# Optimization experiments

Measured on AMD Instinct MI355X. Metric: run time of the kernel, lower is better.

Reference implementation:

```python
import jax, jax.numpy as jnp
import numpy as np

N_NODES = 50000
N_EDGES = 800000
N_IN = 96
N_HID = 96
N_CLS = 16
P_DROP = 0.5


def setup_inputs() -> dict:
    key = jax.random.key(0)
    ks = jax.random.split(key, 10)
    return {
        "features": jax.random.normal(ks[0], (N_NODES, N_IN), dtype=jnp.float32),
        "edge_weight": jax.random.uniform(ks[1], (N_EDGES,), dtype=jnp.float32),
        "src": jax.random.randint(ks[2], (N_EDGES,), 0, N_NODES),
        "dst": jax.random.randint(ks[3], (N_EDGES,), 0, N_NODES),
        "W0": jax.random.normal(ks[4], (N_IN, N_HID), dtype=jnp.float32) / np.sqrt(N_IN).astype(np.float32),
        "b0": jnp.zeros((N_HID,), dtype=jnp.float32),
        "W1": jax.random.normal(ks[5], (N_HID, N_HID), dtype=jnp.float32) / np.sqrt(N_HID).astype(np.float32),
        "b1": jnp.zeros((N_HID,), dtype=jnp.float32),
        "W2": jax.random.normal(ks[6], (N_HID, N_CLS), dtype=jnp.float32) / np.sqrt(N_HID).astype(np.float32),
        "b2": jnp.zeros((N_CLS,), dtype=jnp.float32),
    }


def reference(features, edge_weight, src, dst, W0, b0, W1, b1, W2, b2):
    N = features.shape[0]
    # Unweighted node degrees (DGL GraphConv norm='both'), clamped to >= 1.
    ones_e = jnp.ones_like(edge_weight)
    out_deg = jnp.clip(jax.ops.segment_sum(ones_e, src, num_segments=N), 1.0)
    in_deg = jnp.clip(jax.ops.segment_sum(ones_e, dst, num_segments=N), 1.0)
    inv_sqrt_out = out_deg ** -0.5  # [N]
    inv_sqrt_in = in_deg ** -0.5    # [N]

    def graph_conv(h, W, b, act):
        h = h * inv_sqrt_out[:, None]
        m = h[src] * edge_weight[:, None]                   # [E, d] gather + edge scale
        agg = jax.ops.segment_sum(m, dst, num_segments=N)   # [N, d] scatter-add
        out = (agg * inv_sqrt_in[:, None]) @ W + b          # D_in^-1/2, then linear + bias
        return act(out) if act is not None else out

    layers = [(W0, b0, jax.nn.relu), (W1, b1, jax.nn.relu), (W2, b2, None)]
    dkey = jax.random.key(42)
    h = features
    for i, (W, b, act) in enumerate(layers):
        keep = jax.random.bernoulli(jax.random.fold_in(dkey, i), 1.0 - P_DROP, h.shape)
        h = jnp.where(keep, h / (1.0 - P_DROP), 0.0)        # dropout p=0.5
        h = graph_conv(h, W, b, act)
    return jax.nn.log_softmax(h, axis=1)
```

## Files before the change

kernel.cpp:

```cpp
#include <hip/hip_runtime.h>
#include <hip/hip_fp16.h>
#include <stdint.h>

#define NNODES 50000
#define NEDGES 800000
#define NHID 96
#define NCLS 16

#define NC 100
#define NR 4
#define EPB (NEDGES / NC)
#define RNODES (NNODES / NR)
#define RWORDS8 (RNODES / 4)
#define NWORDS8 (NNODES / 4)
#define SCANB ((NWORDS8 + 255) / 256)
#define FILLBLKS (NC * NR)
#define NDROP4 ((NNODES * NHID / 4 + 255) / 256)

__host__ __device__ inline void tf2x32(uint32_t k0, uint32_t k1, uint32_t x0, uint32_t x1,
                                       uint32_t& o0, uint32_t& o1) {
  uint32_t k2 = k0 ^ k1 ^ 0x1BD11BDAu;
#define TFROT(v, r) (((v) << (r)) | ((v) >> (32 - (r))))
#define TFR(r) { x0 += x1; x1 = TFROT(x1, r); x1 ^= x0; }
  x0 += k0; x1 += k1;
  TFR(13) TFR(15) TFR(26) TFR(6)
  x0 += k1; x1 += k2 + 1u;
  TFR(17) TFR(29) TFR(16) TFR(24)
  x0 += k2; x1 += k0 + 2u;
  TFR(13) TFR(15) TFR(26) TFR(6)
  x0 += k0; x1 += k1 + 3u;
  TFR(17) TFR(29) TFR(16) TFR(24)
  x0 += k1; x1 += k2 + 4u;
  TFR(13) TFR(15) TFR(26) TFR(6)
  x0 += k2; x1 += k0 + 5u;
  o0 = x0; o1 = x1;
#undef TFR
#undef TFROT
}

__device__ inline bool keep_bit(uint32_t k0, uint32_t k1, uint32_t j) {
  uint32_t o0, o1;
  tf2x32(k0, k1, 0u, j, o0, o1);
  return (((o0 ^ o1) >> 31) == 0u);
}

__global__ __launch_bounds__(256) void hist_kernel(
    const int* __restrict__ src, const int* __restrict__ dst,
    uint32_t* __restrict__ slabD, uint32_t* __restrict__ slabS,
    uint32_t* __restrict__ flags) {
  __shared__ uint32_t HD[RWORDS8];
  __shared__ uint32_t HS[RWORDS8];
  const int tid = threadIdx.x, b = blockIdx.x;
  if (b == 0 && tid < SCANB) flags[tid] = 0;
  const int c = b / NR, r = b - c * NR;
  const int e0 = c * EPB, e1 = e0 + EPB;
  const int nbase = r * RNODES;
  for (int w = tid; w < RWORDS8; w += 256) { HD[w] = 0; HS[w] = 0; }
  __syncthreads();
  int e = e0 + tid;
  for (; e + 768 < e1; e += 1024) {
    int d0 = dst[e] - nbase,       d1 = dst[e + 256] - nbase;
    int d2 = dst[e + 512] - nbase, d3 = dst[e + 768] - nbase;
    int s0 = src[e] - nbase,       s1 = src[e + 256] - nbase;
    int s2 = src[e + 512] - nbase, s3 = src[e + 768] - nbase;
    if ((unsigned)d0 < (unsigned)RNODES) atomicAdd(&HD[d0 >> 2], 1u << ((d0 & 3) * 8));
    if ((unsigned)d1 < (unsigned)RNODES) atomicAdd(&HD[d1 >> 2], 1u << ((d1 & 3) * 8));
    if ((unsigned)d2 < (unsigned)RNODES) atomicAdd(&HD[d2 >> 2], 1u << ((d2 & 3) * 8));
    if ((unsigned)d3 < (unsigned)RNODES) atomicAdd(&HD[d3 >> 2], 1u << ((d3 & 3) * 8));
    if ((unsigned)s0 < (unsigned)RNODES) atomicAdd(&HS[s0 >> 2], 1u << ((s0 & 3) * 8));
    if ((unsigned)s1 < (unsigned)RNODES) atomicAdd(&HS[s1 >> 2], 1u << ((s1 & 3) * 8));
    if ((unsigned)s2 < (unsigned)RNODES) atomicAdd(&HS[s2 >> 2], 1u << ((s2 & 3) * 8));
    if ((unsigned)s3 < (unsigned)RNODES) atomicAdd(&HS[s3 >> 2], 1u << ((s3 & 3) * 8));
  }
  for (; e < e1; e += 256) {
    int d = dst[e] - nbase;
    if ((unsigned)d < (unsigned)RNODES) atomicAdd(&HD[d >> 2], 1u << ((d & 3) * 8));
    int s = src[e] - nbase;
    if ((unsigned)s < (unsigned)RNODES) atomicAdd(&HS[s >> 2], 1u << ((s & 3) * 8));
  }
  __syncthreads();
  uint32_t* dpD = slabD + (size_t)b * RWORDS8;
  uint32_t* dpS = slabS + (size_t)b * RWORDS8;
  for (int w = tid; w < RWORDS8; w += 256) { dpD[w] = HD[w]; dpS[w] = HS[w]; }
}

__global__ __launch_bounds__(256) void reduce_scan_kernel(
    const uint32_t* __restrict__ slabD, const uint32_t* __restrict__ slabS,
    float* __restrict__ inv_o, float* __restrict__ inv_i,
    uint32_t* __restrict__ rel8, int* __restrict__ row_ptr,
    uint32_t* __restrict__ flags) {
  __shared__ int lds[256];
  __shared__ int base_s;
  const int tid = threadIdx.x, b = blockIdx.x;
  const int gw = b * 256 + tid;
  uint32_t runD = 0, runS = 0;
  int n0 = 0;
  if (gw < NWORDS8) {
    int r = gw / RWORDS8, lw = gw - r * RWORDS8;
    n0 = r * RNODES + 4 * lw;
#pragma unroll 4
    for (int c = 0; c < NC; ++c) {
      rel8[(size_t)c * NWORDS8 + gw] = runD;
      runD += slabD[(size_t)(c * NR + r) * RWORDS8 + lw];
      runS += slabS[(size_t)(c * NR + r) * RWORDS8 + lw];
    }
  }
  const int d0 = runD & 0xFF, d1 = (runD >> 8) & 0xFF,
            d2 = (runD >> 16) & 0xFF, d3 = runD >> 24;
  const int tsum = d0 + d1 + d2 + d3;
  lds[tid] = tsum;
  __syncthreads();
  for (int off = 1; off < 256; off <<= 1) {
    int t = (tid >= off) ? lds[tid - off] : 0;
    __syncthreads();
    lds[tid] += t;
    __syncthreads();
  }
  const int incl = lds[tid];
  if (tid == 255) atomicExch(&flags[b], 0x80000000u | (uint32_t)lds[255]);
  if (tid < 64) {
    uint32_t part = 0;
    if (tid < b) {
      uint32_t v;
      do { v = atomicAdd(&flags[tid], 0u); } while (!(v & 0x80000000u));
      part = v & 0x7FFFFFFFu;
    }
#pragma unroll
    for (int off = 32; off > 0; off >>= 1)
      part += __shfl_down((unsigned)part, off, 64);
    if (tid == 0) base_s = (int)part;
  }
  __syncthreads();
  const int base = base_s;
  if (gw < NWORDS8) {
    int excl = base + incl - tsum;
    *(int4*)(row_ptr + n0) = make_int4(excl, excl + d0, excl + d0 + d1, excl + d0 + d1 + d2);
    *(float4*)(inv_i + n0) = make_float4(
        rsqrtf(fmaxf((float)d0, 1.0f)), rsqrtf(fmaxf((float)d1, 1.0f)),
        rsqrtf(fmaxf((float)d2, 1.0f)), rsqrtf(fmaxf((float)d3, 1.0f)));
    int o0 = runS & 0xFF, o1 = (runS >> 8) & 0xFF, o2 = (runS >> 16) & 0xFF, o3 = runS >> 24;
    *(float4*)(inv_o + n0) = make_float4(
        rsqrtf(fmaxf((float)o0, 1.0f)), rsqrtf(fmaxf((float)o1, 1.0f)),
        rsqrtf(fmaxf((float)o2, 1.0f)), rsqrtf(fmaxf((float)o3, 1.0f)));
    if (gw == NWORDS8 - 1) row_ptr[NNODES] = NEDGES;
  }
}

__global__ __launch_bounds__(256) void fill_drop_kernel(
    const int* __restrict__ src, const int* __restrict__ dst, const float* __restrict__ ew,
    const uint32_t* __restrict__ rel8, const int* __restrict__ row_ptr,
    uint32_t* __restrict__ csr,
    const float* __restrict__ h, const float* __restrict__ inv_o,
    float* __restrict__ X, uint32_t k0, uint32_t k1) {
  __shared__ uint32_t H[RWORDS8];
  const int tid = threadIdx.x, b = blockIdx.x;
  if (b >= FILLBLKS) {
    int j = ((b - FILLBLKS) * 256 + tid) * 4;
    if (j < NNODES * NHID) {
      int n = j / NHID;
      float4 hv = *(const float4*)(h + j);
      float sc = 2.0f * inv_o[n];
      float4 o;
      o.x = keep_bit(k0, k1, (uint32_t)(j + 0)) ? hv.x * sc : 0.0f;
      o.y = keep_bit(k0, k1, (uint32_t)(j + 1)) ? hv.y * sc : 0.0f;
      o.z = keep_bit(k0, k1, (uint32_t)(j + 2)) ? hv.z * sc : 0.0f;
      o.w = keep_bit(k0, k1, (uint32_t)(j + 3)) ? hv.w * sc : 0.0f;
      *(float4*)(X + j) = o;
    }
    return;
  }
  const int c = b / NR, r = b - c * NR;
  const int e0 = c * EPB, e1 = e0 + EPB;
  const int nbase = r * RNODES;
  const uint32_t* rel = rel8 + (size_t)c * NWORDS8;
  for (int w = tid; w < RWORDS8; w += 256) H[w] = 0;
  __syncthreads();
  int e = e0 + tid;
  for (; e + 256 < e1; e += 512) {
    int da = dst[e], db = dst[e + 256];
    int sa = src[e], sb = src[e + 256];
    float wa = ew[e], wb = ew[e + 256];
    int la = da - nbase, lb = db - nbase;
    bool ia = (unsigned)la < (unsigned)RNODES;
    bool ib = (unsigned)lb < (unsigned)RNODES;
    if (ia) {
      int sh = (la & 3) * 8;
      uint32_t old = atomicAdd(&H[la >> 2], 1u << sh);
      int rank = (int)((old >> sh) & 0xFFu);
      int rel_v = (int)((rel[da >> 2] >> sh) & 0xFFu);
      int pos = row_ptr[da] + rel_v + rank;
      if ((unsigned)pos < (unsigned)NEDGES) {
        uint32_t v = ((uint32_t)sa << 16) | (uint32_t)__half_as_ushort(__float2half_rn(wa));
        __builtin_nontemporal_store(v, &csr[pos]);
      }
    }
    if (ib) {
      int sh = (lb & 3) * 8;
      uint32_t old = atomicAdd(&H[lb >> 2], 1u << sh);
      int rank = (int)((old >> sh) & 0xFFu);
      int rel_v = (int)((rel[db >> 2] >> sh) & 0xFFu);
      int pos = row_ptr[db] + rel_v + rank;
      if ((unsigned)pos < (unsigned)NEDGES) {
        uint32_t v = ((uint32_t)sb << 16) | (uint32_t)__half_as_ushort(__float2half_rn(wb));
        __builtin_nontemporal_store(v, &csr[pos]);
      }
    }
  }
  for (; e < e1; e += 256) {
    int d = dst[e];
    int ld = d - nbase;
    if ((unsigned)ld < (unsigned)RNODES) {
      int sh = (ld & 3) * 8;
      uint32_t old = atomicAdd(&H[ld >> 2], 1u << sh);
      int rank = (int)((old >> sh) & 0xFFu);
      int rel_v = (int)((rel[d >> 2] >> sh) & 0xFFu);
      int pos = row_ptr[d] + rel_v + rank;
      if ((unsigned)pos < (unsigned)NEDGES) {
        uint32_t v = ((uint32_t)src[e] << 16) | (uint32_t)__half_as_ushort(__float2half_rn(ew[e]));
        __builtin_nontemporal_store(v, &csr[pos]);
      }
    }
  }
}

__global__ __launch_bounds__(256) void gemm96_kernel(
    const float* __restrict__ X, const float* __restrict__ W, __half* __restrict__ Yh) {
  __shared__ float Wl[96 * 96];
  const int tid = threadIdx.x;
  {
    const float4* Wg = (const float4*)W;
    float4* Ws = (float4*)Wl;
#pragma unroll
    for (int i = 0; i < 9; ++i)
      Ws[tid + i * 256] = Wg[tid + i * 256];
  }
  __syncthreads();

  const int cg = tid & 7;
  const int rq = tid >> 3;
  const int row0 = blockIdx.x * 128 + rq * 4;
  const int c0 = cg * 12;

  float acc[4][12];
#pragma unroll
  for (int r = 0; r < 4; ++r)
#pragma unroll
    for (int c = 0; c < 12; ++c) acc[r][c] = 0.f;

  const float* xr[4];
#pragma unroll
  for (int r = 0; r < 4; ++r) {
    int rr = row0 + r; if (rr > NNODES - 1) rr = NNODES - 1;
    xr[r] = X + (size_t)rr * 96;
  }

  for (int k = 0; k < 96; k += 4) {
    float4 x4[4];
#pragma unroll
    for (int r = 0; r < 4; ++r) x4[r] = *(const float4*)(xr[r] + k);
#pragma unroll
    for (int kk = 0; kk < 4; ++kk) {
      const float4* wp = (const float4*)(Wl + (k + kk) * 96 + c0);
      float4 w0 = wp[0], w1 = wp[1], w2 = wp[2];
      float xv[4] = { (&x4[0].x)[kk], (&x4[1].x)[kk], (&x4[2].x)[kk], (&x4[3].x)[kk] };
#pragma unroll
      for (int r = 0; r < 4; ++r) {
        acc[r][0]  += xv[r] * w0.x; acc[r][1]  += xv[r] * w0.y;
        acc[r][2]  += xv[r] * w0.z; acc[r][3]  += xv[r] * w0.w;
        acc[r][4]  += xv[r] * w1.x; acc[r][5]  += xv[r] * w1.y;
        acc[r][6]  += xv[r] * w1.z; acc[r][7]  += xv[r] * w1.w;
        acc[r][8]  += xv[r] * w2.x; acc[r][9]  += xv[r] * w2.y;
        acc[r][10] += xv[r] * w2.z; acc[r][11] += xv[r] * w2.w;
      }
    }
  }

#pragma unroll
  for (int r = 0; r < 4; ++r) {
    int rr = row0 + r;
    if (rr < NNODES) {
      __half2* hp = (__half2*)(Yh + (size_t)rr * 96 + c0);
#pragma unroll
      for (int c = 0; c < 6; ++c)
        hp[c] = __floats2half2_rn(acc[r][2 * c], acc[r][2 * c + 1]);
    }
  }
}

__global__ __launch_bounds__(256) void gemm16_kernel(
    const float* __restrict__ X, const float* __restrict__ W, __half* __restrict__ Y2h) {
  __shared__ float Wl[96 * 16];
  const int tid = threadIdx.x;
  {
    const float4* Wg = (const float4*)W;
    float4* Ws = (float4*)Wl;
    for (int i = tid; i < 384; i += 256) Ws[i] = Wg[i];
  }
  __syncthreads();

  const int row0 = blockIdx.x * 512 + tid * 2;
  const float* xr[2];
#pragma unroll
  for (int r = 0; r < 2; ++r) {
    int rr = row0 + r; if (rr > NNODES - 1) rr = NNODES - 1;
    xr[r] = X + (size_t)rr * 96;
  }

  float acc[2][16];
#pragma unroll
  for (int r = 0; r < 2; ++r)
#pragma unroll
    for (int c = 0; c < 16; ++c) acc[r][c] = 0.f;

  for (int k = 0; k < 96; k += 4) {
    float4 x4[2];
#pragma unroll
    for (int r = 0; r < 2; ++r) x4[r] = *(const float4*)(xr[r] + k);
#pragma unroll
    for (int kk = 0; kk < 4; ++kk) {
      const float4* wp = (const float4*)(Wl + (k + kk) * 16);
      float4 w0 = wp[0], w1 = wp[1], w2 = wp[2], w3 = wp[3];
#pragma unroll
      for (int r = 0; r < 2; ++r) {
        float xv = (&x4[r].x)[kk];
        acc[r][0]  += xv * w0.x; acc[r][1]  += xv * w0.y;
        acc[r][2]  += xv * w0.z; acc[r][3]  += xv * w0.w;
        acc[r][4]  += xv * w1.x; acc[r][5]  += xv * w1.y;
        acc[r][6]  += xv * w1.z; acc[r][7]  += xv * w1.w;
        acc[r][8]  += xv * w2.x; acc[r][9]  += xv * w2.y;
        acc[r][10] += xv * w2.z; acc[r][11] += xv * w2.w;
        acc[r][12] += xv * w3.x; acc[r][13] += xv * w3.y;
        acc[r][14] += xv * w3.z; acc[r][15] += xv * w3.w;
      }
    }
  }

#pragma unroll
  for (int r = 0; r < 2; ++r) {
    int rr = row0 + r;
    if (rr < NNODES) {
      __half2* hp = (__half2*)(Y2h + (size_t)rr * 16);
#pragma unroll
      for (int c = 0; c < 8; ++c)
        hp[c] = __floats2half2_rn(acc[r][2 * c], acc[r][2 * c + 1]);
    }
  }
}

#define ACC16(u0, u1, wt) { \
  float2 g0 = __half22float2(*(__half2*)&u0.x); \
  float2 g1 = __half22float2(*(__half2*)&u0.y); \
  float2 g2 = __half22float2(*(__half2*)&u0.z); \
  float2 g3 = __half22float2(*(__half2*)&u0.w); \
  float2 g4 = __half22float2(*(__half2*)&u1.x); \
  float2 g5 = __half22float2(*(__half2*)&u1.y); \
  float2 g6 = __half22float2(*(__half2*)&u1.z); \
  float2 g7 = __half22float2(*(__half2*)&u1.w); \
  acc[0]  += g0.x * wt; acc[1]  += g0.y * wt; \
  acc[2]  += g1.x * wt; acc[3]  += g1.y * wt; \
  acc[4]  += g2.x * wt; acc[5]  += g2.y * wt; \
  acc[6]  += g3.x * wt; acc[7]  += g3.y * wt; \
  acc[8]  += g4.x * wt; acc[9]  += g4.y * wt; \
  acc[10] += g5.x * wt; acc[11] += g5.y * wt; \
  acc[12] += g6.x * wt; acc[13] += g6.y * wt; \
  acc[14] += g7.x * wt; acc[15] += g7.y * wt; }

__global__ __launch_bounds__(256) void gather96_drop_kernel(
    const __half* __restrict__ Yh, const uint32_t* __restrict__ csr,
    const int* __restrict__ row_ptr, const float* __restrict__ inv_in,
    const float* __restrict__ inv_o, const float* __restrict__ bias,
    float* __restrict__ Xn, uint32_t k0, uint32_t k1) {
  int tid = blockIdx.x * 256 + threadIdx.x;
  int n = tid / 6;
  int q = tid - n * 6;
  if (n >= NNODES) return;
  int beg = row_ptr[n], end = row_ptr[n + 1];
  float acc[16];
#pragma unroll
  for (int i = 0; i < 16; ++i) acc[i] = 0.f;

  int p = beg;
  for (; p + 4 <= end; p += 4) {
    uint32_t pa = csr[p], pb = csr[p + 1], pc = csr[p + 2], pd = csr[p + 3];
    int s0 = pa >> 16, s1 = pb >> 16, s2 = pc >> 16, s3 = pd >> 16;
    if (s0 >= NNODES) s0 = 0;
    if (s1 >= NNODES) s1 = 0;
    if (s2 >= NNODES) s2 = 0;
    if (s3 >= NNODES) s3 = 0;
    float w0 = __half2float(__ushort_as_half((unsigned short)(pa & 0xFFFFu)));
    float w1 = __half2float(__ushort_as_half((unsigned short)(pb & 0xFFFFu)));
    float w2 = __half2float(__ushort_as_half((unsigned short)(pc & 0xFFFFu)));
    float w3 = __half2float(__ushort_as_half((unsigned short)(pd & 0xFFFFu)));
    const uint4* y0 = (const uint4*)(Yh + (size_t)s0 * 96 + q * 16);
    const uint4* y1 = (const uint4*)(Yh + (size_t)s1 * 96 + q * 16);
    const uint4* y2 = (const uint4*)(Yh + (size_t)s2 * 96 + q * 16);
    const uint4* y3 = (const uint4*)(Yh + (size_t)s3 * 96 + q * 16);
    uint4 a0 = y0[0], a1 = y0[1];
    uint4 b0 = y1[0], b1 = y1[1];
    uint4 c0 = y2[0], c1 = y2[1];
    uint4 d0 = y3[0], d1 = y3[1];
    ACC16(a0, a1, w0)
    ACC16(b0, b1, w1)
    ACC16(c0, c1, w2)
    ACC16(d0, d1, w3)
  }
  for (; p + 2 <= end; p += 2) {
    uint32_t pa = csr[p], pb = csr[p + 1];
    int s0 = pa >> 16, s1 = pb >> 16;
    if (s0 >= NNODES) s0 = 0;
    if (s1 >= NNODES) s1 = 0;
    float w0 = __half2float(__ushort_as_half((unsigned short)(pa & 0xFFFFu)));
    float w1 = __half2float(__ushort_as_half((unsigned short)(pb & 0xFFFFu)));
    const uint4* y0 = (const uint4*)(Yh + (size_t)s0 * 96 + q * 16);
    const uint4* y1 = (const uint4*)(Yh + (size_t)s1 * 96 + q * 16);
    uint4 a0 = y0[0], a1 = y0[1];
    uint4 b0 = y1[0], b1 = y1[1];
    ACC16(a0, a1, w0)
    ACC16(b0, b1, w1)
  }
  if (p < end) {
    uint32_t pa = csr[p];
    int s0 = pa >> 16;
    if (s0 >= NNODES) s0 = 0;
    float w0 = __half2float(__ushort_as_half((unsigned short)(pa & 0xFFFFu)));
    const uint4* y0 = (const uint4*)(Yh + (size_t)s0 * 96 + q * 16);
    uint4 a0 = y0[0], a1 = y0[1];
    ACC16(a0, a1, w0)
  }

  float iv = inv_in[n];
  float sc = 2.0f * inv_o[n];
  const float* bp = bias + q * 16;
  float o[16];
#pragma unroll
  for (int i = 0; i < 16; ++i)
    o[i] = fmaxf(acc[i] * iv + bp[i], 0.f) * sc;
  uint32_t jb = (uint32_t)(n * 96 + q * 16);
#pragma unroll
  for (int i = 0; i < 16; ++i)
    o[i] = keep_bit(k0, k1, jb + i) ? o[i] : 0.f;
  float* xp = Xn + (size_t)n * 96 + q * 16;
  *(float4*)(xp + 0)  = make_float4(o[0], o[1], o[2], o[3]);
  *(float4*)(xp + 4)  = make_float4(o[4], o[5], o[6], o[7]);
  *(float4*)(xp + 8)  = make_float4(o[8], o[9], o[10], o[11]);
  *(float4*)(xp + 12) = make_float4(o[12], o[13], o[14], o[15]);
}

__global__ __launch_bounds__(256) void gather16_lsm_kernel(
    const __half* __restrict__ Y2h, const uint32_t* __restrict__ csr,
    const int* __restrict__ row_ptr, const float* __restrict__ inv_in,
    const float* __restrict__ b2, float* __restrict__ out) {
  int n = blockIdx.x * 256 + threadIdx.x;
  if (n >= NNODES) return;
  int beg = row_ptr[n], end = row_ptr[n + 1];
  float acc[16];
#pragma unroll
  for (int i = 0; i < 16; ++i) acc[i] = 0.f;

  int p = beg;
  for (; p + 2 <= end; p += 2) {
    uint32_t pa = csr[p], pb = csr[p + 1];
    int sa = pa >> 16, sb = pb >> 16;
    if (sa >= NNODES) sa = 0;
    if (sb >= NNODES) sb = 0;
    float wa = __half2float(__ushort_as_half((unsigned short)(pa & 0xFFFFu)));
    float wb = __half2float(__ushort_as_half((unsigned short)(pb & 0xFFFFu)));
    const uint4* ya = (const uint4*)(Y2h + (size_t)sa * 16);
    const uint4* yb = (const uint4*)(Y2h + (size_t)sb * 16);
    uint4 a0 = ya[0], a1 = ya[1];
    uint4 b0 = yb[0], b1 = yb[1];
    ACC16(a0, a1, wa)
    ACC16(b0, b1, wb)
  }
  if (p < end) {
    uint32_t pa = csr[p];
    int sa = pa >> 16;
    if (sa >= NNODES) sa = 0;
    float wa = __half2float(__ushort_as_half((unsigned short)(pa & 0xFFFFu)));
    const uint4* ya = (const uint4*)(Y2h + (size_t)sa * 16);
    uint4 a0 = ya[0], a1 = ya[1];
    ACC16(a0, a1, wa)
  }

  float iv = inv_in[n];
  float v[16];
#pragma unroll
  for (int i = 0; i < 16; ++i) v[i] = acc[i] * iv + b2[i];
  float m = v[0];
#pragma unroll
  for (int i = 1; i < 16; i++) m = fmaxf(m, v[i]);
  float s = 0.f;
#pragma unroll
  for (int i = 0; i < 16; i++) s += expf(v[i] - m);
  float ls = logf(s);
  float* orow = out + (size_t)n * 16;
#pragma unroll
  for (int i = 0; i < 16; i++) orow[i] = v[i] - m - ls;
}

extern "C" void kernel_launch(void* const* d_in, const int* in_sizes, int n_in,
                              void* d_out, int out_size, void* d_ws, size_t ws_size,
                              hipStream_t stream) {
  const float* feat = (const float*)d_in[0];
  const float* ew   = (const float*)d_in[1];
  const int*   src  = (const int*)d_in[2];
  const int*   dst  = (const int*)d_in[3];
  const float* W0   = (const float*)d_in[4];
  const float* b0   = (const float*)d_in[5];
  const float* W1   = (const float*)d_in[6];
  const float* b1   = (const float*)d_in[7];
  const float* W2   = (const float*)d_in[8];
  const float* b2   = (const float*)d_in[9];
  float* out = (float*)d_out;

  char* base = (char*)d_ws;
  size_t off = 0;
  auto take = [&](size_t nbytes) {
    void* q = base + off;
    off += (nbytes + 255) & ~(size_t)255;
    return q;
  };
  uint32_t* flags   = (uint32_t*)take((size_t)SCANB * 4);
  int*      row_ptr = (int*)take((size_t)(NNODES + 1) * 4);
  float*    inv_o   = (float*)take((size_t)NNODES * 4);
  float*    inv_i   = (float*)take((size_t)NNODES * 4);
  uint32_t* slabD   = (uint32_t*)take((size_t)NC * NR * RWORDS8 * 4);
  uint32_t* slabS   = (uint32_t*)take((size_t)NC * NR * RWORDS8 * 4);
  uint32_t* rel8    = (uint32_t*)take((size_t)NC * NWORDS8 * 4);
  uint32_t* csr     = (uint32_t*)take((size_t)NEDGES * 4);
  float*    X       = (float*)take((size_t)NNODES * NHID * 4);
  __half*   Yh      = (__half*)take((size_t)NNODES * NHID * 2);
  __half*   Y2h     = (__half*)take((size_t)NNODES * NCLS * 2);
  (void)ws_size; (void)in_sizes; (void)n_in; (void)out_size;

  uint32_t k[3][2];
  for (uint32_t i = 0; i < 3; i++) tf2x32(0u, 42u, 0u, i, k[i][0], k[i][1]);

  hist_kernel<<<FILLBLKS, 256, 0, stream>>>(src, dst, slabD, slabS, flags);
  reduce_scan_kernel<<<SCANB, 256, 0, stream>>>(slabD, slabS, inv_o, inv_i, rel8, row_ptr, flags);
  fill_drop_kernel<<<FILLBLKS + NDROP4, 256, 0, stream>>>(
      src, dst, ew, rel8, row_ptr, csr, feat, inv_o, X, k[0][0], k[0][1]);

  const int G96  = (NNODES + 127) / 128;
  const int G16  = (NNODES + 511) / 512;
  const int GGD  = (NNODES * 6 + 255) / 256;

  gemm96_kernel<<<G96, 256, 0, stream>>>(X, W0, Yh);
  gather96_drop_kernel<<<GGD, 256, 0, stream>>>(Yh, csr, row_ptr, inv_i, inv_o, b0, X, k[1][0], k[1][1]);
  gemm96_kernel<<<G96, 256, 0, stream>>>(X, W1, Yh);
  gather96_drop_kernel<<<GGD, 256, 0, stream>>>(Yh, csr, row_ptr, inv_i, inv_o, b1, X, k[2][0], k[2][1]);
  gemm16_kernel<<<G16, 256, 0, stream>>>(X, W2, Y2h);
  gather16_lsm_kernel<<<(NNODES + 255) / 256, 256, 0, stream>>>(Y2h, csr, row_ptr, inv_i, b2, out);
}
```

Before: 278.0 us.

## Record per-edge ranks in histogram pass and parallelize CSR fill across edges

The histogram kernel now saves each edge's intra-chunk rank (returned by the LDS atomic) into a byte array. The CSR fill stage no longer replays the atomics in 400 blocks that each scan an edge chunk. It instead runs fully parallel, with one thread per four edges using vectorized loads to compute positions directly. This removes the redundant second atomic pass and the low-parallelism chunk scans, at the cost of an extra 800KB byte array written and read, plus regular rather than nontemporal stores.

```diff
diff --git a/kernel.cpp b/kernel.cpp
--- a/kernel.cpp
+++ b/kernel.cpp
@@ -14,7 +14,9 @@
 #define RWORDS8 (RNODES / 4)
 #define NWORDS8 (NNODES / 4)
 #define SCANB ((NWORDS8 + 255) / 256)
-#define FILLBLKS (NC * NR)
+#define HISTBLKS (NC * NR)
+#define FEPT 4
+#define FILLB2 ((NEDGES / FEPT + 255) / 256)
 #define NDROP4 ((NNODES * NHID / 4 + 255) / 256)
 
 __host__ __device__ inline void tf2x32(uint32_t k0, uint32_t k1, uint32_t x0, uint32_t x1,
@@ -47,7 +49,7 @@
 __global__ __launch_bounds__(256) void hist_kernel(
     const int* __restrict__ src, const int* __restrict__ dst,
     uint32_t* __restrict__ slabD, uint32_t* __restrict__ slabS,
-    uint32_t* __restrict__ flags) {
+    uint8_t* __restrict__ rank8, uint32_t* __restrict__ flags) {
   __shared__ uint32_t HD[RWORDS8];
   __shared__ uint32_t HS[RWORDS8];
   const int tid = threadIdx.x, b = blockIdx.x;
@@ -63,10 +65,26 @@
     int d2 = dst[e + 512] - nbase, d3 = dst[e + 768] - nbase;
     int s0 = src[e] - nbase,       s1 = src[e + 256] - nbase;
     int s2 = src[e + 512] - nbase, s3 = src[e + 768] - nbase;
-    if ((unsigned)d0 < (unsigned)RNODES) atomicAdd(&HD[d0 >> 2], 1u << ((d0 & 3) * 8));
-    if ((unsigned)d1 < (unsigned)RNODES) atomicAdd(&HD[d1 >> 2], 1u << ((d1 & 3) * 8));
-    if ((unsigned)d2 < (unsigned)RNODES) atomicAdd(&HD[d2 >> 2], 1u << ((d2 & 3) * 8));
-    if ((unsigned)d3 < (unsigned)RNODES) atomicAdd(&HD[d3 >> 2], 1u << ((d3 & 3) * 8));
+    if ((unsigned)d0 < (unsigned)RNODES) {
+      int sh = (d0 & 3) * 8;
+      uint32_t old = atomicAdd(&HD[d0 >> 2], 1u << sh);
+      rank8[e] = (uint8_t)((old >> sh) & 0xFFu);
+    }
+    if ((unsigned)d1 < (unsigned)RNODES) {
+      int sh = (d1 & 3) * 8;
+      uint32_t old = atomicAdd(&HD[d1 >> 2], 1u << sh);
+      rank8[e + 256] = (uint8_t)((old >> sh) & 0xFFu);
+    }
+    if ((unsigned)d2 < (unsigned)RNODES) {
+      int sh = (d2 & 3) * 8;
+      uint32_t old = atomicAdd(&HD[d2 >> 2], 1u << sh);
+      rank8[e + 512] = (uint8_t)((old >> sh) & 0xFFu);
+    }
+    if ((unsigned)d3 < (unsigned)RNODES) {
+      int sh = (d3 & 3) * 8;
+      uint32_t old = atomicAdd(&HD[d3 >> 2], 1u << sh);
+      rank8[e + 768] = (uint8_t)((old >> sh) & 0xFFu);
+    }
     if ((unsigned)s0 < (unsigned)RNODES) atomicAdd(&HS[s0 >> 2], 1u << ((s0 & 3) * 8));
     if ((unsigned)s1 < (unsigned)RNODES) atomicAdd(&HS[s1 >> 2], 1u << ((s1 & 3) * 8));
     if ((unsigned)s2 < (unsigned)RNODES) atomicAdd(&HS[s2 >> 2], 1u << ((s2 & 3) * 8));
@@ -74,7 +92,11 @@
   }
   for (; e < e1; e += 256) {
     int d = dst[e] - nbase;
-    if ((unsigned)d < (unsigned)RNODES) atomicAdd(&HD[d >> 2], 1u << ((d & 3) * 8));
+    if ((unsigned)d < (unsigned)RNODES) {
+      int sh = (d & 3) * 8;
+      uint32_t old = atomicAdd(&HD[d >> 2], 1u << sh);
+      rank8[e] = (uint8_t)((old >> sh) & 0xFFu);
+    }
     int s = src[e] - nbase;
     if ((unsigned)s < (unsigned)RNODES) atomicAdd(&HS[s >> 2], 1u << ((s & 3) * 8));
   }
@@ -148,78 +170,45 @@
 
 __global__ __launch_bounds__(256) void fill_drop_kernel(
     const int* __restrict__ src, const int* __restrict__ dst, const float* __restrict__ ew,
-    const uint32_t* __restrict__ rel8, const int* __restrict__ row_ptr,
-    uint32_t* __restrict__ csr,
+    const uint8_t* __restrict__ rank8, const uint32_t* __restrict__ rel8,
+    const int* __restrict__ row_ptr, uint32_t* __restrict__ csr,
     const float* __restrict__ h, const float* __restrict__ inv_o,
     float* __restrict__ X, uint32_t k0, uint32_t k1) {
-  __shared__ uint32_t H[RWORDS8];
-  const int tid = threadIdx.x, b = blockIdx.x;
-  if (b >= FILLBLKS) {
-    int j = ((b - FILLBLKS) * 256 + tid) * 4;
-    if (j < NNODES * NHID) {
-      int n = j / NHID;
-      float4 hv = *(const float4*)(h + j);
-      float sc = 2.0f * inv_o[n];
-      float4 o;
-      o.x = keep_bit(k0, k1, (uint32_t)(j + 0)) ? hv.x * sc : 0.0f;
-      o.y = keep_bit(k0, k1, (uint32_t)(j + 1)) ? hv.y * sc : 0.0f;
-      o.z = keep_bit(k0, k1, (uint32_t)(j + 2)) ? hv.z * sc : 0.0f;
-      o.w = keep_bit(k0, k1, (uint32_t)(j + 3)) ? hv.w * sc : 0.0f;
-      *(float4*)(X + j) = o;
+  const int bi = blockIdx.x;
+  if (bi < FILLB2) {
+    int t = bi * 256 + threadIdx.x;
+    int e = t * 4;
+    if (e >= NEDGES) return;
+    int4 d4 = *(const int4*)(dst + e);
+    int4 s4 = *(const int4*)(src + e);
+    float4 w4 = *(const float4*)(ew + e);
+    uint32_t r4 = *(const uint32_t*)(rank8 + e);
+    const uint32_t* rel = rel8 + (size_t)(e / EPB) * NWORDS8;
+#pragma unroll
+    for (int k = 0; k < 4; ++k) {
+      int d = (&d4.x)[k];
+      int s = (&s4.x)[k];
+      float w = (&w4.x)[k];
+      int rk = (int)((r4 >> (k * 8)) & 0xFFu);
+      int sh = (d & 3) * 8;
+      int rel_v = (int)((rel[d >> 2] >> sh) & 0xFFu);
+      int pos = row_ptr[d] + rel_v + rk;
+      uint32_t v = ((uint32_t)s << 16) | (uint32_t)__half_as_ushort(__float2half_rn(w));
+      if ((unsigned)pos < (unsigned)NEDGES) csr[pos] = v;
     }
     return;
   }
-  const int c = b / NR, r = b - c * NR;
-  const int e0 = c * EPB, e1 = e0 + EPB;
-  const int nbase = r * RNODES;
-  const uint32_t* rel = rel8 + (size_t)c * NWORDS8;
-  for (int w = tid; w < RWORDS8; w += 256) H[w] = 0;
-  __syncthreads();
-  int e = e0 + tid;
-  for (; e + 256 < e1; e += 512) {
-    int da = dst[e], db = dst[e + 256];
-    int sa = src[e], sb = src[e + 256];
-    float wa = ew[e], wb = ew[e + 256];
-    int la = da - nbase, lb = db - nbase;
-    bool ia = (unsigned)la < (unsigned)RNODES;
-    bool ib = (unsigned)lb < (unsigned)RNODES;
-    if (ia) {
-      int sh = (la & 3) * 8;
-      uint32_t old = atomicAdd(&H[la >> 2], 1u << sh);
-      int rank = (int)((old >> sh) & 0xFFu);
-      int rel_v = (int)((rel[da >> 2] >> sh) & 0xFFu);
-      int pos = row_ptr[da] + rel_v + rank;
-      if ((unsigned)pos < (unsigned)NEDGES) {
-        uint32_t v = ((uint32_t)sa << 16) | (uint32_t)__half_as_ushort(__float2half_rn(wa));
-        __builtin_nontemporal_store(v, &csr[pos]);
-      }
-    }
-    if (ib) {
-      int sh = (lb & 3) * 8;
-      uint32_t old = atomicAdd(&H[lb >> 2], 1u << sh);
-      int rank = (int)((old >> sh) & 0xFFu);
-      int rel_v = (int)((rel[db >> 2] >> sh) & 0xFFu);
-      int pos = row_ptr[db] + rel_v + rank;
-      if ((unsigned)pos < (unsigned)NEDGES) {
-        uint32_t v = ((uint32_t)sb << 16) | (uint32_t)__half_as_ushort(__float2half_rn(wb));
-        __builtin_nontemporal_store(v, &csr[pos]);
-      }
-    }
-  }
-  for (; e < e1; e += 256) {
-    int d = dst[e];
-    int ld = d - nbase;
-    if ((unsigned)ld < (unsigned)RNODES) {
-      int sh = (ld & 3) * 8;
-      uint32_t old = atomicAdd(&H[ld >> 2], 1u << sh);
-      int rank = (int)((old >> sh) & 0xFFu);
-      int rel_v = (int)((rel[d >> 2] >> sh) & 0xFFu);
-      int pos = row_ptr[d] + rel_v + rank;
-      if ((unsigned)pos < (unsigned)NEDGES) {
-        uint32_t v = ((uint32_t)src[e] << 16) | (uint32_t)__half_as_ushort(__float2half_rn(ew[e]));
-        __builtin_nontemporal_store(v, &csr[pos]);
-      }
-    }
+  int j = ((bi - FILLB2) * 256 + threadIdx.x) * 4;
+  if (j < NNODES * NHID) {
+    int n = j / NHID;
+    float4 hv = *(const float4*)(h + j);
+    float sc = 2.0f * inv_o[n];
+    float4 o;
+    o.x = keep_bit(k0, k1, (uint32_t)(j + 0)) ? hv.x * sc : 0.0f;
+    o.y = keep_bit(k0, k1, (uint32_t)(j + 1)) ? hv.y * sc : 0.0f;
+    o.z = keep_bit(k0, k1, (uint32_t)(j + 2)) ? hv.z * sc : 0.0f;
+    o.w = keep_bit(k0, k1, (uint32_t)(j + 3)) ? hv.w * sc : 0.0f;
+    *(float4*)(X + j) = o;
   }
 }
 
@@ -527,6 +516,7 @@
   uint32_t* slabD   = (uint32_t*)take((size_t)NC * NR * RWORDS8 * 4);
   uint32_t* slabS   = (uint32_t*)take((size_t)NC * NR * RWORDS8 * 4);
   uint32_t* rel8    = (uint32_t*)take((size_t)NC * NWORDS8 * 4);
+  uint8_t*  rank8   = (uint8_t*)take((size_t)NEDGES);
   uint32_t* csr     = (uint32_t*)take((size_t)NEDGES * 4);
   float*    X       = (float*)take((size_t)NNODES * NHID * 4);
   __half*   Yh      = (__half*)take((size_t)NNODES * NHID * 2);
@@ -536,10 +526,10 @@
   uint32_t k[3][2];
   for (uint32_t i = 0; i < 3; i++) tf2x32(0u, 42u, 0u, i, k[i][0], k[i][1]);
 
-  hist_kernel<<<FILLBLKS, 256, 0, stream>>>(src, dst, slabD, slabS, flags);
+  hist_kernel<<<HISTBLKS, 256, 0, stream>>>(src, dst, slabD, slabS, rank8, flags);
   reduce_scan_kernel<<<SCANB, 256, 0, stream>>>(slabD, slabS, inv_o, inv_i, rel8, row_ptr, flags);
-  fill_drop_kernel<<<FILLBLKS + NDROP4, 256, 0, stream>>>(
-      src, dst, ew, rel8, row_ptr, csr, feat, inv_o, X, k[0][0], k[0][1]);
+  fill_drop_kernel<<<FILLB2 + NDROP4, 256, 0, stream>>>(
+      src, dst, ew, rank8, rel8, row_ptr, csr, feat, inv_o, X, k[0][0], k[0][1]);
 
   const int G96  = (NNODES + 127) / 128;
   const int G16  = (NNODES + 511) / 512;
```

Result: no change. 276.2 us (-0.7%).
